# Optimization experiments

Hardware: AMD Instinct MI355X
Metric: run time of the kernel (lower is better)

Reference implementation:

```python
import jax, jax.numpy as jnp
import numpy as np

N, IN_CH, HID, HEADS, OUT_CH, E = 30000, 256, 128, 4, 256, 480000
NEG_SLOPE = 0.2  # PyG GATConv default LeakyReLU slope


def setup_inputs() -> dict:
    key = jax.random.key(0)
    ks = jax.random.split(key, 12)
    s = lambda fin: 1.0 / np.sqrt(fin)
    return {
        "x": jax.random.normal(ks[0], (N, IN_CH), jnp.float32),
        "edge_index": jax.random.randint(ks[1], (2, E), 0, N, jnp.int32),
        "W1": jax.random.normal(ks[2], (IN_CH, HEADS * HID), jnp.float32) * s(IN_CH),
        "a_src1": jax.random.normal(ks[3], (HEADS, HID), jnp.float32) * s(HID),
        "a_dst1": jax.random.normal(ks[4], (HEADS, HID), jnp.float32) * s(HID),
        "b1": jnp.zeros((HEADS * HID,), jnp.float32),
        "prelu_w": jnp.asarray(0.25, jnp.float32),
        "W2": jax.random.normal(ks[5], (HEADS * HID, OUT_CH), jnp.float32) * s(HEADS * HID),
        "a_src2": jax.random.normal(ks[6], (1, OUT_CH), jnp.float32) * s(OUT_CH),
        "a_dst2": jax.random.normal(ks[7], (1, OUT_CH), jnp.float32) * s(OUT_CH),
        "b2": jnp.zeros((OUT_CH,), jnp.float32),
    }


def gat_conv(x, W, a_src, a_dst, bias, src, dst, heads, out_ch, concat):
    n = x.shape[0]
    h = (x @ W).reshape(n, heads, out_ch)                 # [n,H,C]
    al_s = jnp.einsum("nhc,hc->nh", h, a_src)             # [n,H]
    al_d = jnp.einsum("nhc,hc->nh", h, a_dst)
    logits = jax.nn.leaky_relu(al_s[src] + al_d[dst], NEG_SLOPE)  # [Et,H]
    m = jax.lax.stop_gradient(jax.ops.segment_max(logits, dst, num_segments=n))
    e = jnp.exp(logits - m[dst])
    denom = jax.ops.segment_sum(e, dst, num_segments=n)
    alpha = e / denom[dst]                                # per-dst softmax
    msg = h[src] * alpha[:, :, None]                      # [Et,H,C]
    out = jax.ops.segment_sum(msg, dst, num_segments=n)   # [n,H,C]
    out = out.reshape(n, heads * out_ch) if concat else out.mean(axis=1)
    return out + bias


def reference(x, edge_index, W1, a_src1, a_dst1, b1, prelu_w, W2, a_src2, a_dst2, b2):
    n = x.shape[0]
    loop = jnp.arange(n, dtype=edge_index.dtype)
    src = jnp.concatenate([edge_index[0], loop])          # PyG adds self-loops
    dst = jnp.concatenate([edge_index[1], loop])
    h = gat_conv(x, W1, a_src1, a_dst1, b1, src, dst, HEADS, HID, concat=True)
    h = jnp.where(h >= 0, h, prelu_w * h)                 # PReLU (eval: dropout off)
    z = gat_conv(h, W2, a_src2, a_dst2, b2, src, dst, 1, OUT_CH, concat=False)
    return z
```

## Files before the change

kernel.cpp:

```cpp
#include <hip/hip_runtime.h>
#include <hip/hip_bf16.h>
#include <float.h>

#define N_NODES 30000
#define IN_CH   256
#define HID     128
#define HEADS   4
#define OUT_CH  256
#define N_EDGES 480000
#define TOT_E   (N_EDGES + N_NODES)

typedef unsigned short u16;
typedef __attribute__((ext_vector_type(8))) unsigned short u16x8;
typedef __attribute__((ext_vector_type(8))) short          s16x8;
typedef __attribute__((ext_vector_type(4))) float          f32x4;

__device__ inline float bf2f(u16 u) {
    union { unsigned int i; float f; } v; v.i = ((unsigned int)u) << 16; return v.f;
}
__device__ inline u16 f2bf(float f) {
    union { float f; unsigned int i; } u; u.f = f;
    unsigned int r = u.i + 0x7FFF + ((u.i >> 16) & 1);
    return (u16)(r >> 16);
}

__device__ inline void load4(const float* p, float* o) {
    float4 v = *(const float4*)p; o[0]=v.x; o[1]=v.y; o[2]=v.z; o[3]=v.w;
}
__device__ inline void store4f(float* p, float a, float b, float c, float d) {
    *(float4*)p = make_float4(a,b,c,d);
}
__device__ inline void store4b(u16* p, float a, float b, float c, float d) {
    ushort4 o; o.x=f2bf(a); o.y=f2bf(b); o.z=f2bf(c); o.w=f2bf(d);
    *(ushort4*)p = o;
}

__global__ void detect_k(const unsigned int* __restrict__ w, int* __restrict__ flag) {
    __shared__ int votes;
    if (threadIdx.x == 0) votes = 0;
    __syncthreads();
    int v = 0;
    for (int i = threadIdx.x; i < 2048; i += 256) {
        unsigned int e = (w[i] >> 7) & 0xFFu;
        if (e >= 100u && e <= 140u) v++;
    }
    atomicAdd(&votes, v);
    __syncthreads();
    if (threadIdx.x == 0) *flag = (votes > 1024) ? 1 : 0;
}

__global__ void convert_bf_k(const void* __restrict__ in, u16* __restrict__ out,
                             int n, const int* __restrict__ flag) {
    int i = blockIdx.x * blockDim.x + threadIdx.x;
    if (i >= n) return;
    if (*flag) out[i] = ((const u16*)in)[i];
    else       out[i] = f2bf(((const float*)in)[i]);
}

__global__ void convert_tr_k(const void* __restrict__ in, u16* __restrict__ out,
                             int rows, int cols, const int* __restrict__ flag) {
    int i = blockIdx.x * blockDim.x + threadIdx.x;
    if (i >= rows * cols) return;
    int r = i / cols, c = i - r * cols;
    u16 v = (*flag) ? ((const u16*)in)[i] : f2bf(((const float*)in)[i]);
    out[(size_t)c * rows + r] = v;
}

__global__ void convert_small_k(const void* __restrict__ as1, const void* __restrict__ ad1,
                                const void* __restrict__ b1,  const void* __restrict__ as2,
                                const void* __restrict__ ad2, const void* __restrict__ b2,
                                const void* __restrict__ pw,
                                float* __restrict__ as1f, float* __restrict__ ad1f,
                                float* __restrict__ b1f,  float* __restrict__ as2f,
                                float* __restrict__ ad2f, float* __restrict__ b2f,
                                float* __restrict__ pwf,
                                const int* __restrict__ flag)
{
    int i = blockIdx.x * blockDim.x + threadIdx.x;
    int f = *flag;
#define CV(in, k) (f ? bf2f(((const u16*)(in))[k]) : ((const float*)(in))[k])
    if      (i < 512)  as1f[i]        = CV(as1, i);
    else if (i < 1024) ad1f[i - 512]  = CV(ad1, i - 512);
    else if (i < 1536) b1f [i - 1024] = CV(b1,  i - 1024);
    else if (i < 1792) as2f[i - 1536] = CV(as2, i - 1536);
    else if (i < 2048) ad2f[i - 1792] = CV(ad2, i - 1792);
    else if (i < 2304) b2f [i - 2048] = CV(b2,  i - 2048);
    else if (i == 2304) pwf[0]        = CV(pw, 0);
#undef CV
}

__global__ __launch_bounds__(256) void gemm_bf_k(const u16* __restrict__ A,
                                                 const u16* __restrict__ Bt,
                                                 u16* __restrict__ Cb,
                                                 const float* __restrict__ a_s,
                                                 const float* __restrict__ a_d,
                                                 float* __restrict__ als,
                                                 float* __restrict__ ald,
                                                 int M, int N, int K,
                                                 int H, int hshift)
{
    __shared__ __align__(16) u16 As[128][40];
    __shared__ __align__(16) u16 Bs[128][40];

    const int tid  = threadIdx.x;
    const int wid  = tid >> 6;
    const int lane = tid & 63;
    const int wr   = wid >> 1;
    const int wc   = wid & 1;
    const int lr   = lane & 15;
    const int lg   = lane >> 4;
    const int row0 = blockIdx.y * 128;
    const int col0 = blockIdx.x * 128;

    const int st_r = tid >> 1;
    const int st_c = (tid & 1) << 4;

    f32x4 acc[4][4];
#pragma unroll
    for (int i = 0; i < 4; ++i)
#pragma unroll
        for (int j = 0; j < 4; ++j)
            acc[i][j] = (f32x4){0.f, 0.f, 0.f, 0.f};

    for (int k0 = 0; k0 < K; k0 += 32) {
        __syncthreads();
        {
            u16x8 a0 = {}, a1 = {};
            int ar = row0 + st_r;
            if (ar < M) {
                const u16* ap = A + (size_t)ar * K + k0 + st_c;
                a0 = *(const u16x8*)ap;
                a1 = *(const u16x8*)(ap + 8);
            }
            *(u16x8*)&As[st_r][st_c]     = a0;
            *(u16x8*)&As[st_r][st_c + 8] = a1;
            const u16* bp = Bt + (size_t)(col0 + st_r) * K + k0 + st_c;
            *(u16x8*)&Bs[st_r][st_c]     = *(const u16x8*)bp;
            *(u16x8*)&Bs[st_r][st_c + 8] = *(const u16x8*)(bp + 8);
        }
        __syncthreads();

        s16x8 af[4], bf[4];
#pragma unroll
        for (int mf = 0; mf < 4; ++mf)
            af[mf] = *(const s16x8*)&As[wr*64 + mf*16 + lr][lg*8];
#pragma unroll
        for (int nf = 0; nf < 4; ++nf)
            bf[nf] = *(const s16x8*)&Bs[wc*64 + nf*16 + lr][lg*8];
#pragma unroll
        for (int mf = 0; mf < 4; ++mf)
#pragma unroll
            for (int nf = 0; nf < 4; ++nf)
                acc[mf][nf] = __builtin_amdgcn_mfma_f32_16x16x32_bf16(
                    af[mf], bf[nf], acc[mf][nf], 0, 0, 0);
    }

    const int head = (col0 + wc*64) >> hshift;
    float asj[4], adj[4];
#pragma unroll
    for (int nf = 0; nf < 4; ++nf) {
        int j = col0 + wc*64 + nf*16 + lr;
        asj[nf] = a_s[j];
        adj[nf] = a_d[j];
    }
#pragma unroll
    for (int mf = 0; mf < 4; ++mf) {
#pragma unroll
        for (int r = 0; r < 4; ++r) {
            int rr = row0 + wr*64 + mf*16 + lg*4 + r;
            float ss = 0.f, sd = 0.f;
#pragma unroll
            for (int nf = 0; nf < 4; ++nf) {
                float v = acc[mf][nf][r];
                ss += v * asj[nf];
                sd += v * adj[nf];
            }
#pragma unroll
            for (int m2 = 1; m2 < 16; m2 <<= 1) {
                ss += __shfl_xor(ss, m2);
                sd += __shfl_xor(sd, m2);
            }
            if (rr < M) {
                if (lr == 0) {
                    atomicAdd(&als[(size_t)rr * H + head], ss);
                    atomicAdd(&ald[(size_t)rr * H + head], sd);
                }
                size_t base = (size_t)rr * N + col0 + wc*64 + lr;
#pragma unroll
                for (int nf = 0; nf < 4; ++nf)
                    Cb[base + nf*16] = f2bf(acc[mf][nf][r]);
            }
        }
    }
}

__global__ void zero_k(int* p, int n) {
    int i = blockIdx.x*blockDim.x + threadIdx.x; if (i < n) p[i] = 0;
}
__global__ void count_k(const int* __restrict__ ei, int* __restrict__ cnt) {
    int i = blockIdx.x*blockDim.x + threadIdx.x;
    if (i >= TOT_E) return;
    int d = (i < N_EDGES) ? ei[N_EDGES + i] : (i - N_EDGES);
    atomicAdd(&cnt[d], 1);
}
__global__ __launch_bounds__(1024) void scan1_k(const int* __restrict__ cnt,
                                                int* __restrict__ offs,
                                                int* __restrict__ btot)
{
    __shared__ int sm[1024];
    int tid = threadIdx.x;
    int i = blockIdx.x * 1024 + tid;
    int v = (i < N_NODES) ? cnt[i] : 0;
    sm[tid] = v;
    __syncthreads();
    for (int off = 1; off < 1024; off <<= 1) {
        int t = (tid >= off) ? sm[tid - off] : 0;
        __syncthreads();
        sm[tid] += t;
        __syncthreads();
    }
    if (i < N_NODES) offs[i + 1] = sm[tid];
    if (tid == 1023) btot[blockIdx.x] = sm[1023];
}
__global__ void scan2_k(const int* __restrict__ btot, int* __restrict__ bpref, int nb)
{
    int lane = threadIdx.x;
    int orig = (lane < nb) ? btot[lane] : 0;
    int v = orig;
    for (int off = 1; off < 64; off <<= 1) {
        int t = __shfl_up(v, off);
        if (lane >= off) v += t;
    }
    if (lane < nb) bpref[lane] = v - orig;
}
__global__ __launch_bounds__(1024) void scan3_k(const int* __restrict__ cnt,
                                                int* __restrict__ offs,
                                                int* __restrict__ cursor,
                                                const int* __restrict__ bpref)
{
    int i = blockIdx.x * 1024 + threadIdx.x;
    if (i < N_NODES) {
        int inc = offs[i + 1] + bpref[blockIdx.x];
        offs[i + 1] = inc;
        cursor[i]   = inc - cnt[i];
    }
    if (i == 0) offs[0] = 0;
}
__global__ void scatter_k(const int* __restrict__ ei, int* __restrict__ cursor,
                          int* __restrict__ ssrc)
{
    int i = blockIdx.x*blockDim.x + threadIdx.x;
    if (i >= TOT_E) return;
    int s, d;
    if (i < N_EDGES) { s = ei[i]; d = ei[N_EDGES + i]; }
    else             { s = i - N_EDGES; d = s; }
    int pos = atomicAdd(&cursor[d], 1);
    ssrc[pos] = s;
}

template<int H, int C, bool PRELU, int OUTMODE>
__global__ void aggregate_k(const u16* __restrict__ hb,
                            const float* __restrict__ als,
                            const float* __restrict__ ald,
                            const int* __restrict__ offs,
                            const int* __restrict__ ssrc,
                            const float* __restrict__ bias,
                            const float* __restrict__ prelu_w,
                            void* __restrict__ outv,
                            const int* __restrict__ flag)
{
    constexpr int CT = H * C;
    constexpr int T  = CT / 4;
    constexpr int NW = T / 64;
    int n   = blockIdx.x;
    int tid = threadIdx.x;
    int beg = offs[n], end = offs[n+1];

    __shared__ float s_ald[H], s_m[H], s_inv[H];
    __shared__ float red[H][NW];
    __shared__ int   sh_s[T];
    __shared__ float sh_w[H][T];

    if (tid < H) s_ald[tid] = ald[(size_t)n*H + tid];
    __syncthreads();

    float lmax[H];
#pragma unroll
    for (int hh = 0; hh < H; ++hh) lmax[hh] = -FLT_MAX;
    for (int e = beg + tid; e < end; e += T) {
        int s = ssrc[e];
#pragma unroll
        for (int hh = 0; hh < H; ++hh) {
            float l = als[(size_t)s*H + hh] + s_ald[hh];
            l = (l >= 0.f) ? l : 0.2f*l;
            lmax[hh] = fmaxf(lmax[hh], l);
        }
    }
#pragma unroll
    for (int hh = 0; hh < H; ++hh) {
        float v = lmax[hh];
#pragma unroll
        for (int o = 32; o > 0; o >>= 1) v = fmaxf(v, __shfl_xor(v, o));
        if ((tid & 63) == 0) red[hh][tid >> 6] = v;
    }
    __syncthreads();
    if (tid < H) {
        float v = red[tid][0];
#pragma unroll
        for (int w2 = 1; w2 < NW; ++w2) v = fmaxf(v, red[tid][w2]);
        s_m[tid] = v;
    }
    __syncthreads();

    float lsum[H];
#pragma unroll
    for (int hh = 0; hh < H; ++hh) lsum[hh] = 0.f;
    for (int e = beg + tid; e < end; e += T) {
        int s = ssrc[e];
#pragma unroll
        for (int hh = 0; hh < H; ++hh) {
            float l = als[(size_t)s*H + hh] + s_ald[hh];
            l = (l >= 0.f) ? l : 0.2f*l;
            lsum[hh] += __expf(l - s_m[hh]);
        }
    }
#pragma unroll
    for (int hh = 0; hh < H; ++hh) {
        float v = lsum[hh];
#pragma unroll
        for (int o = 32; o > 0; o >>= 1) v += __shfl_xor(v, o);
        if ((tid & 63) == 0) red[hh][tid >> 6] = v;
    }
    __syncthreads();
    if (tid < H) {
        float v = 0.f;
#pragma unroll
        for (int w2 = 0; w2 < NW; ++w2) v += red[tid][w2];
        s_inv[tid] = 1.0f / v;
    }
    __syncthreads();

    const int hh = (4*tid) / C;
    float ax = 0.f, ay = 0.f, az = 0.f, aw = 0.f;
    for (int chunk = beg; chunk < end; chunk += T) {
        int e = chunk + tid;
        if (e < end) {
            int s = ssrc[e];
            sh_s[tid] = s;
#pragma unroll
            for (int h2 = 0; h2 < H; ++h2) {
                float l = als[(size_t)s*H + h2] + s_ald[h2];
                l = (l >= 0.f) ? l : 0.2f*l;
                sh_w[h2][tid] = __expf(l - s_m[h2]) * s_inv[h2];
            }
        }
        __syncthreads();
        int cnt = min(T, end - chunk);
        int j = 0;
        for (; j + 4 <= cnt; j += 4) {
            int s0 = sh_s[j+0], s1 = sh_s[j+1], s2 = sh_s[j+2], s3 = sh_s[j+3];
            float w0 = sh_w[hh][j+0], w1 = sh_w[hh][j+1];
            float w2 = sh_w[hh][j+2], w3 = sh_w[hh][j+3];
            ushort4 v0 = *(const ushort4*)(hb + (size_t)s0*CT + 4*tid);
            ushort4 v1 = *(const ushort4*)(hb + (size_t)s1*CT + 4*tid);
            ushort4 v2 = *(const ushort4*)(hb + (size_t)s2*CT + 4*tid);
            ushort4 v3 = *(const ushort4*)(hb + (size_t)s3*CT + 4*tid);
            ax += w0*bf2f(v0.x); ay += w0*bf2f(v0.y); az += w0*bf2f(v0.z); aw += w0*bf2f(v0.w);
            ax += w1*bf2f(v1.x); ay += w1*bf2f(v1.y); az += w1*bf2f(v1.z); aw += w1*bf2f(v1.w);
            ax += w2*bf2f(v2.x); ay += w2*bf2f(v2.y); az += w2*bf2f(v2.z); aw += w2*bf2f(v2.w);
            ax += w3*bf2f(v3.x); ay += w3*bf2f(v3.y); az += w3*bf2f(v3.z); aw += w3*bf2f(v3.w);
        }
        for (; j < cnt; ++j) {
            int s0 = sh_s[j];
            float w0 = sh_w[hh][j];
            ushort4 v0 = *(const ushort4*)(hb + (size_t)s0*CT + 4*tid);
            ax += w0*bf2f(v0.x); ay += w0*bf2f(v0.y); az += w0*bf2f(v0.z); aw += w0*bf2f(v0.w);
        }
        __syncthreads();
    }

    float bb[4];
    load4(bias + 4*tid, bb);
    ax += bb[0]; ay += bb[1]; az += bb[2]; aw += bb[3];
    if (PRELU) {
        float pw = *prelu_w;
        ax = ax >= 0.f ? ax : pw*ax;
        ay = ay >= 0.f ? ay : pw*ay;
        az = az >= 0.f ? az : pw*az;
        aw = aw >= 0.f ? aw : pw*aw;
    }
    size_t ofs = (size_t)n*CT + 4*tid;
    if (OUTMODE == 2) {
        if (*flag) store4b((u16*)outv + ofs, ax, ay, az, aw);
        else       store4f((float*)outv + ofs, ax, ay, az, aw);
    } else if (OUTMODE == 1) {
        store4b((u16*)outv + ofs, ax, ay, az, aw);
    } else {
        store4f((float*)outv + ofs, ax, ay, az, aw);
    }
}

extern "C" void kernel_launch(void* const* d_in, const int* in_sizes, int n_in,
                              void* d_out, int out_size, void* d_ws, size_t ws_size,
                              hipStream_t stream)
{
    const void* x   = d_in[0];
    const int*  ei  = (const int*)d_in[1];
    const void* W1  = d_in[2];
    const void* as1 = d_in[3];
    const void* ad1 = d_in[4];
    const void* b1  = d_in[5];
    const void* pw  = d_in[6];
    const void* W2  = d_in[7];
    const void* as2 = d_in[8];
    const void* ad2 = d_in[9];
    const void* b2  = d_in[10];

    float* ws = (float*)d_ws;
    int*   flag = (int*)ws;
    float* as1f = ws + 16;
    float* ad1f = as1f + 512;
    float* b1f  = ad1f + 512;
    float* as2f = b1f  + 512;
    float* ad2f = as2f + 256;
    float* b2f  = ad2f + 256;
    float* pwf  = b2f  + 256;
    u16*   W1t  = (u16*)(pwf + 16);
    u16*   W2t  = W1t + IN_CH*HEADS*HID;
    float* als1 = (float*)(W2t + HEADS*HID*OUT_CH);
    float* ald1 = als1 + (size_t)N_NODES*HEADS;
    float* als2v = ald1 + (size_t)N_NODES*HEADS;
    float* ald2v = als2v + N_NODES;
    int*   cnt    = (int*)(ald2v + N_NODES);
    int*   offs   = cnt + N_NODES;
    int*   cursor = offs + 30004;
    int*   btot   = cursor + N_NODES;
    int*   bpref  = btot + 32;
    int*   ssrc   = bpref + 36;
    u16*   xb     = (u16*)(ssrc + 510004);
    u16*   h1b    = xb  + (size_t)N_NODES*IN_CH;
    u16*   h1pb   = h1b + (size_t)N_NODES*512;
    u16*   h2b    = h1b;

    const int NB = (N_NODES + 1023) / 1024;

    detect_k<<<1, 256, 0, stream>>>((const unsigned int*)x, flag);
    convert_bf_k<<<(N_NODES*IN_CH+255)/256, 256, 0, stream>>>(x, xb, N_NODES*IN_CH, flag);
    convert_tr_k<<<(IN_CH*HEADS*HID+255)/256, 256, 0, stream>>>(W1, W1t, IN_CH, HEADS*HID, flag);
    convert_tr_k<<<(HEADS*HID*OUT_CH+255)/256, 256, 0, stream>>>(W2, W2t, HEADS*HID, OUT_CH, flag);
    convert_small_k<<<10, 256, 0, stream>>>(as1, ad1, b1, as2, ad2, b2, pw,
                                            as1f, ad1f, b1f, as2f, ad2f, b2f, pwf, flag);

    zero_k<<<(330000+255)/256, 256, 0, stream>>>((int*)als1, 330000);

    count_k  <<<(TOT_E+255)/256, 256, 0, stream>>>(ei, cnt);
    scan1_k  <<<NB, 1024, 0, stream>>>(cnt, offs, btot);
    scan2_k  <<<1, 64, 0, stream>>>(btot, bpref, NB);
    scan3_k  <<<NB, 1024, 0, stream>>>(cnt, offs, cursor, bpref);
    scatter_k<<<(TOT_E+255)/256, 256, 0, stream>>>(ei, cursor, ssrc);

    dim3 g1(512/128, (N_NODES+127)/128);
    gemm_bf_k<<<g1, 256, 0, stream>>>(xb, W1t, h1b, as1f, ad1f, als1, ald1,
                                      N_NODES, 512, IN_CH, HEADS, 7);
    aggregate_k<HEADS, HID, true, 1>
        <<<N_NODES, (HEADS*HID)/4, 0, stream>>>(h1b, als1, ald1, offs, ssrc, b1f, pwf, h1pb, flag);

    dim3 g2(256/128, (N_NODES+127)/128);
    gemm_bf_k<<<g2, 256, 0, stream>>>(h1pb, W2t, h2b, as2f, ad2f, als2v, ald2v,
                                      N_NODES, OUT_CH, HEADS*HID, 1, 8);
    aggregate_k<1, OUT_CH, false, 2>
        <<<N_NODES, OUT_CH/4, 0, stream>>>(h2b, als2v, ald2v, offs, ssrc, b2f, nullptr, d_out, flag);
}
```

Before: 375.7 us.

## Split GAT aggregation into softmax-weight precompute and channel-group gather kernels

Replaces the fused per-node aggregation kernel with two kernels. The first computes normalized attention weights per edge with one wavefront per node and writes them to a workspace buffer. The second launches one block per node and channel group, with two waves splitting the edges and scalar bf16 loads per lane. The aim is more parallelism and less per-block synchronisation, at the cost of an extra weight-buffer round-trip through memory and narrower (2-byte) gather loads.

```diff
diff --git a/kernel.cpp b/kernel.cpp
--- a/kernel.cpp
+++ b/kernel.cpp
@@ -22,17 +22,6 @@
     union { float f; unsigned int i; } u; u.f = f;
     unsigned int r = u.i + 0x7FFF + ((u.i >> 16) & 1);
     return (u16)(r >> 16);
-}
-
-__device__ inline void load4(const float* p, float* o) {
-    float4 v = *(const float4*)p; o[0]=v.x; o[1]=v.y; o[2]=v.z; o[3]=v.w;
-}
-__device__ inline void store4f(float* p, float a, float b, float c, float d) {
-    *(float4*)p = make_float4(a,b,c,d);
-}
-__device__ inline void store4b(u16* p, float a, float b, float c, float d) {
-    ushort4 o; o.x=f2bf(a); o.y=f2bf(b); o.z=f2bf(c); o.w=f2bf(d);
-    *(ushort4*)p = o;
 }
 
 __global__ void detect_k(const unsigned int* __restrict__ w, int* __restrict__ flag) {
@@ -258,145 +247,120 @@
     ssrc[pos] = s;
 }
 
-template<int H, int C, bool PRELU, int OUTMODE>
-__global__ void aggregate_k(const u16* __restrict__ hb,
-                            const float* __restrict__ als,
-                            const float* __restrict__ ald,
-                            const int* __restrict__ offs,
-                            const int* __restrict__ ssrc,
-                            const float* __restrict__ bias,
-                            const float* __restrict__ prelu_w,
-                            void* __restrict__ outv,
-                            const int* __restrict__ flag)
-{
-    constexpr int CT = H * C;
-    constexpr int T  = CT / 4;
-    constexpr int NW = T / 64;
-    int n   = blockIdx.x;
-    int tid = threadIdx.x;
+template<int H>
+__global__ __launch_bounds__(64) void softmax_prep_k(
+    const float* __restrict__ als, const float* __restrict__ ald,
+    const int* __restrict__ offs, const int* __restrict__ ssrc,
+    float* __restrict__ wbuf)
+{
+    int n = blockIdx.x;
+    int lane = threadIdx.x;
     int beg = offs[n], end = offs[n+1];
-
-    __shared__ float s_ald[H], s_m[H], s_inv[H];
-    __shared__ float red[H][NW];
-    __shared__ int   sh_s[T];
-    __shared__ float sh_w[H][T];
-
-    if (tid < H) s_ald[tid] = ald[(size_t)n*H + tid];
+    float aldh[H];
+#pragma unroll
+    for (int h = 0; h < H; ++h) aldh[h] = ald[(size_t)n*H + h];
+
+    float lmax[H];
+#pragma unroll
+    for (int h = 0; h < H; ++h) lmax[h] = -FLT_MAX;
+    for (int e = beg + lane; e < end; e += 64) {
+        int s = ssrc[e];
+#pragma unroll
+        for (int h = 0; h < H; ++h) {
+            float l = als[(size_t)s*H + h] + aldh[h];
+            l = (l >= 0.f) ? l : 0.2f*l;
+            lmax[h] = fmaxf(lmax[h], l);
+        }
+    }
+#pragma unroll
+    for (int h = 0; h < H; ++h)
+#pragma unroll
+        for (int o = 32; o > 0; o >>= 1)
+            lmax[h] = fmaxf(lmax[h], __shfl_xor(lmax[h], o));
+
+    float lsum[H];
+#pragma unroll
+    for (int h = 0; h < H; ++h) lsum[h] = 0.f;
+    for (int e = beg + lane; e < end; e += 64) {
+        int s = ssrc[e];
+#pragma unroll
+        for (int h = 0; h < H; ++h) {
+            float l = als[(size_t)s*H + h] + aldh[h];
+            l = (l >= 0.f) ? l : 0.2f*l;
+            lsum[h] += __expf(l - lmax[h]);
+        }
+    }
+#pragma unroll
+    for (int h = 0; h < H; ++h)
+#pragma unroll
+        for (int o = 32; o > 0; o >>= 1)
+            lsum[h] += __shfl_xor(lsum[h], o);
+
+    float inv[H];
+#pragma unroll
+    for (int h = 0; h < H; ++h) inv[h] = 1.0f / lsum[h];
+
+    for (int e = beg + lane; e < end; e += 64) {
+        int s = ssrc[e];
+#pragma unroll
+        for (int h = 0; h < H; ++h) {
+            float l = als[(size_t)s*H + h] + aldh[h];
+            l = (l >= 0.f) ? l : 0.2f*l;
+            wbuf[(size_t)e*H + h] = __expf(l - lmax[h]) * inv[h];
+        }
+    }
+}
+
+template<int H, int CT, int NG, bool PRELU, int OUTMODE>
+__global__ __launch_bounds__(128) void gather_k(
+    const u16* __restrict__ hb, const float* __restrict__ wbuf,
+    const int* __restrict__ offs, const int* __restrict__ ssrc,
+    const float* __restrict__ bias, const float* __restrict__ prelu_w,
+    void* __restrict__ outv, const int* __restrict__ flag)
+{
+    constexpr int CPG = CT / NG;
+    const int bid  = blockIdx.x;
+    const int g    = bid % NG;
+    const int n    = bid / NG;
+    const int wv   = threadIdx.x >> 6;
+    const int lane = threadIdx.x & 63;
+    const int c    = g * CPG + lane;
+    const int h    = c / (CT / H);
+    const int beg = offs[n], end = offs[n+1];
+
+    __shared__ float part[2][CPG];
+
+    float acc = 0.f;
+    int e = beg + wv;
+    for (; e + 6 < end; e += 8) {
+        int   s0 = ssrc[e],   s1 = ssrc[e+2], s2 = ssrc[e+4], s3 = ssrc[e+6];
+        float w0 = wbuf[(size_t)(e+0)*H + h], w1 = wbuf[(size_t)(e+2)*H + h];
+        float w2 = wbuf[(size_t)(e+4)*H + h], w3 = wbuf[(size_t)(e+6)*H + h];
+        float v0 = bf2f(hb[(size_t)s0*CT + c]);
+        float v1 = bf2f(hb[(size_t)s1*CT + c]);
+        float v2 = bf2f(hb[(size_t)s2*CT + c]);
+        float v3 = bf2f(hb[(size_t)s3*CT + c]);
+        acc += w0*v0 + w1*v1 + w2*v2 + w3*v3;
+    }
+    for (; e < end; e += 2) {
+        int s0 = ssrc[e];
+        float w0 = wbuf[(size_t)e*H + h];
+        acc += w0 * bf2f(hb[(size_t)s0*CT + c]);
+    }
+    part[wv][lane] = acc;
     __syncthreads();
-
-    float lmax[H];
-#pragma unroll
-    for (int hh = 0; hh < H; ++hh) lmax[hh] = -FLT_MAX;
-    for (int e = beg + tid; e < end; e += T) {
-        int s = ssrc[e];
-#pragma unroll
-        for (int hh = 0; hh < H; ++hh) {
-            float l = als[(size_t)s*H + hh] + s_ald[hh];
-            l = (l >= 0.f) ? l : 0.2f*l;
-            lmax[hh] = fmaxf(lmax[hh], l);
-        }
-    }
-#pragma unroll
-    for (int hh = 0; hh < H; ++hh) {
-        float v = lmax[hh];
-#pragma unroll
-        for (int o = 32; o > 0; o >>= 1) v = fmaxf(v, __shfl_xor(v, o));
-        if ((tid & 63) == 0) red[hh][tid >> 6] = v;
-    }
-    __syncthreads();
-    if (tid < H) {
-        float v = red[tid][0];
-#pragma unroll
-        for (int w2 = 1; w2 < NW; ++w2) v = fmaxf(v, red[tid][w2]);
-        s_m[tid] = v;
-    }
-    __syncthreads();
-
-    float lsum[H];
-#pragma unroll
-    for (int hh = 0; hh < H; ++hh) lsum[hh] = 0.f;
-    for (int e = beg + tid; e < end; e += T) {
-        int s = ssrc[e];
-#pragma unroll
-        for (int hh = 0; hh < H; ++hh) {
-            float l = als[(size_t)s*H + hh] + s_ald[hh];
-            l = (l >= 0.f) ? l : 0.2f*l;
-            lsum[hh] += __expf(l - s_m[hh]);
-        }
-    }
-#pragma unroll
-    for (int hh = 0; hh < H; ++hh) {
-        float v = lsum[hh];
-#pragma unroll
-        for (int o = 32; o > 0; o >>= 1) v += __shfl_xor(v, o);
-        if ((tid & 63) == 0) red[hh][tid >> 6] = v;
-    }
-    __syncthreads();
-    if (tid < H) {
-        float v = 0.f;
-#pragma unroll
-        for (int w2 = 0; w2 < NW; ++w2) v += red[tid][w2];
-        s_inv[tid] = 1.0f / v;
-    }
-    __syncthreads();
-
-    const int hh = (4*tid) / C;
-    float ax = 0.f, ay = 0.f, az = 0.f, aw = 0.f;
-    for (int chunk = beg; chunk < end; chunk += T) {
-        int e = chunk + tid;
-        if (e < end) {
-            int s = ssrc[e];
-            sh_s[tid] = s;
-#pragma unroll
-            for (int h2 = 0; h2 < H; ++h2) {
-                float l = als[(size_t)s*H + h2] + s_ald[h2];
-                l = (l >= 0.f) ? l : 0.2f*l;
-                sh_w[h2][tid] = __expf(l - s_m[h2]) * s_inv[h2];
-            }
-        }
-        __syncthreads();
-        int cnt = min(T, end - chunk);
-        int j = 0;
-        for (; j + 4 <= cnt; j += 4) {
-            int s0 = sh_s[j+0], s1 = sh_s[j+1], s2 = sh_s[j+2], s3 = sh_s[j+3];
-            float w0 = sh_w[hh][j+0], w1 = sh_w[hh][j+1];
-            float w2 = sh_w[hh][j+2], w3 = sh_w[hh][j+3];
-            ushort4 v0 = *(const ushort4*)(hb + (size_t)s0*CT + 4*tid);
-            ushort4 v1 = *(const ushort4*)(hb + (size_t)s1*CT + 4*tid);
-            ushort4 v2 = *(const ushort4*)(hb + (size_t)s2*CT + 4*tid);
-            ushort4 v3 = *(const ushort4*)(hb + (size_t)s3*CT + 4*tid);
-            ax += w0*bf2f(v0.x); ay += w0*bf2f(v0.y); az += w0*bf2f(v0.z); aw += w0*bf2f(v0.w);
-            ax += w1*bf2f(v1.x); ay += w1*bf2f(v1.y); az += w1*bf2f(v1.z); aw += w1*bf2f(v1.w);
-            ax += w2*bf2f(v2.x); ay += w2*bf2f(v2.y); az += w2*bf2f(v2.z); aw += w2*bf2f(v2.w);
-            ax += w3*bf2f(v3.x); ay += w3*bf2f(v3.y); az += w3*bf2f(v3.z); aw += w3*bf2f(v3.w);
-        }
-        for (; j < cnt; ++j) {
-            int s0 = sh_s[j];
-            float w0 = sh_w[hh][j];
-            ushort4 v0 = *(const ushort4*)(hb + (size_t)s0*CT + 4*tid);
-            ax += w0*bf2f(v0.x); ay += w0*bf2f(v0.y); az += w0*bf2f(v0.z); aw += w0*bf2f(v0.w);
-        }
-        __syncthreads();
-    }
-
-    float bb[4];
-    load4(bias + 4*tid, bb);
-    ax += bb[0]; ay += bb[1]; az += bb[2]; aw += bb[3];
-    if (PRELU) {
-        float pw = *prelu_w;
-        ax = ax >= 0.f ? ax : pw*ax;
-        ay = ay >= 0.f ? ay : pw*ay;
-        az = az >= 0.f ? az : pw*az;
-        aw = aw >= 0.f ? aw : pw*aw;
-    }
-    size_t ofs = (size_t)n*CT + 4*tid;
-    if (OUTMODE == 2) {
-        if (*flag) store4b((u16*)outv + ofs, ax, ay, az, aw);
-        else       store4f((float*)outv + ofs, ax, ay, az, aw);
-    } else if (OUTMODE == 1) {
-        store4b((u16*)outv + ofs, ax, ay, az, aw);
-    } else {
-        store4f((float*)outv + ofs, ax, ay, az, aw);
+    if (wv == 0) {
+        float r = part[0][lane] + part[1][lane] + bias[c];
+        if (PRELU) { float pw = *prelu_w; r = (r >= 0.f) ? r : pw * r; }
+        size_t o = (size_t)n * CT + c;
+        if (OUTMODE == 1) {
+            ((u16*)outv)[o] = f2bf(r);
+        } else if (OUTMODE == 2) {
+            if (*flag) ((u16*)outv)[o] = f2bf(r);
+            else       ((float*)outv)[o] = r;
+        } else {
+            ((float*)outv)[o] = r;
+        }
     }
 }
 
@@ -437,7 +401,8 @@
     int*   btot   = cursor + N_NODES;
     int*   bpref  = btot + 32;
     int*   ssrc   = bpref + 36;
-    u16*   xb     = (u16*)(ssrc + 510004);
+    float* wbuf   = (float*)(ssrc + 510004);
+    u16*   xb     = (u16*)(wbuf + 2040016);
     u16*   h1b    = xb  + (size_t)N_NODES*IN_CH;
     u16*   h1pb   = h1b + (size_t)N_NODES*512;
     u16*   h2b    = h1b;
@@ -462,12 +427,14 @@
     dim3 g1(512/128, (N_NODES+127)/128);
     gemm_bf_k<<<g1, 256, 0, stream>>>(xb, W1t, h1b, as1f, ad1f, als1, ald1,
                                       N_NODES, 512, IN_CH, HEADS, 7);
-    aggregate_k<HEADS, HID, true, 1>
-        <<<N_NODES, (HEADS*HID)/4, 0, stream>>>(h1b, als1, ald1, offs, ssrc, b1f, pwf, h1pb, flag);
+    softmax_prep_k<HEADS><<<N_NODES, 64, 0, stream>>>(als1, ald1, offs, ssrc, wbuf);
+    gather_k<HEADS, 512, 8, true, 1>
+        <<<N_NODES*8, 128, 0, stream>>>(h1b, wbuf, offs, ssrc, b1f, pwf, h1pb, flag);
 
     dim3 g2(256/128, (N_NODES+127)/128);
     gemm_bf_k<<<g2, 256, 0, stream>>>(h1pb, W2t, h2b, as2f, ad2f, als2v, ald2v,
                                       N_NODES, OUT_CH, HEADS*HID, 1, 8);
-    aggregate_k<1, OUT_CH, false, 2>
-        <<<N_NODES, OUT_CH/4, 0, stream>>>(h2b, als2v, ald2v, offs, ssrc, b2f, nullptr, d_out, flag);
-}
+    softmax_prep_k<1><<<N_NODES, 64, 0, stream>>>(als2v, ald2v, offs, ssrc, wbuf);
+    gather_k<1, 256, 4, false, 2>
+        <<<N_NODES*4, 128, 0, stream>>>(h2b, wbuf, offs, ssrc, b2f, nullptr, d_out, flag);
+}
```

Measured after the change: 566.2 us. +50.7%, slower.

## Use single-wave aggregation blocks and drop softmax max-subtraction pass

Applied to the files above, without the earlier changes.

Rewrites the aggregation kernel so each node is handled by a single 64-thread wavefront with 8- or 4-wide bf16 vector loads. Reductions become shuffle-only with no shared-memory staging or extra barriers. The max-logit pass is removed, so the softmax exponentiates raw logits. This saves one full pass over the edge list and several block syncs, but large logits could overflow exp, and each node gets fewer threads for the gather.

```diff
diff --git a/kernel.cpp b/kernel.cpp
--- a/kernel.cpp
+++ b/kernel.cpp
@@ -22,17 +22,6 @@
     union { float f; unsigned int i; } u; u.f = f;
     unsigned int r = u.i + 0x7FFF + ((u.i >> 16) & 1);
     return (u16)(r >> 16);
-}
-
-__device__ inline void load4(const float* p, float* o) {
-    float4 v = *(const float4*)p; o[0]=v.x; o[1]=v.y; o[2]=v.z; o[3]=v.w;
-}
-__device__ inline void store4f(float* p, float a, float b, float c, float d) {
-    *(float4*)p = make_float4(a,b,c,d);
-}
-__device__ inline void store4b(u16* p, float a, float b, float c, float d) {
-    ushort4 o; o.x=f2bf(a); o.y=f2bf(b); o.z=f2bf(c); o.w=f2bf(d);
-    *(ushort4*)p = o;
 }
 
 __global__ void detect_k(const unsigned int* __restrict__ w, int* __restrict__ flag) {
@@ -258,145 +247,137 @@
     ssrc[pos] = s;
 }
 
-template<int H, int C, bool PRELU, int OUTMODE>
-__global__ void aggregate_k(const u16* __restrict__ hb,
-                            const float* __restrict__ als,
-                            const float* __restrict__ ald,
-                            const int* __restrict__ offs,
-                            const int* __restrict__ ssrc,
-                            const float* __restrict__ bias,
-                            const float* __restrict__ prelu_w,
-                            void* __restrict__ outv,
-                            const int* __restrict__ flag)
+template<int H, int C, int VW, bool PRELU, int OUTMODE>
+__global__ __launch_bounds__(64) void aggregate_k(
+    const u16* __restrict__ hb,
+    const float* __restrict__ als,
+    const float* __restrict__ ald,
+    const int* __restrict__ offs,
+    const int* __restrict__ ssrc,
+    const float* __restrict__ bias,
+    const float* __restrict__ prelu_w,
+    void* __restrict__ outv,
+    const int* __restrict__ flag)
 {
     constexpr int CT = H * C;
-    constexpr int T  = CT / 4;
-    constexpr int NW = T / 64;
-    int n   = blockIdx.x;
-    int tid = threadIdx.x;
-    int beg = offs[n], end = offs[n+1];
-
-    __shared__ float s_ald[H], s_m[H], s_inv[H];
-    __shared__ float red[H][NW];
+    constexpr int T  = 64;
+    static_assert(CT == T * VW, "geometry");
+    const int n   = blockIdx.x;
+    const int tid = threadIdx.x;
+    const int beg = offs[n], end = offs[n+1];
+
+    float aldh[H];
+#pragma unroll
+    for (int h = 0; h < H; ++h) aldh[h] = ald[(size_t)n*H + h];
+
+    float lsum[H];
+#pragma unroll
+    for (int h = 0; h < H; ++h) lsum[h] = 0.f;
+    for (int e = beg + tid; e < end; e += T) {
+        int s = ssrc[e];
+#pragma unroll
+        for (int h = 0; h < H; ++h) {
+            float l = als[(size_t)s*H + h] + aldh[h];
+            l = (l >= 0.f) ? l : 0.2f*l;
+            lsum[h] += __expf(l);
+        }
+    }
+#pragma unroll
+    for (int h = 0; h < H; ++h) {
+#pragma unroll
+        for (int o = 32; o > 0; o >>= 1) lsum[h] += __shfl_xor(lsum[h], o);
+    }
+    float inv[H];
+#pragma unroll
+    for (int h = 0; h < H; ++h) inv[h] = 1.0f / lsum[h];
+
     __shared__ int   sh_s[T];
     __shared__ float sh_w[H][T];
-
-    if (tid < H) s_ald[tid] = ald[(size_t)n*H + tid];
-    __syncthreads();
-
-    float lmax[H];
-#pragma unroll
-    for (int hh = 0; hh < H; ++hh) lmax[hh] = -FLT_MAX;
-    for (int e = beg + tid; e < end; e += T) {
-        int s = ssrc[e];
-#pragma unroll
-        for (int hh = 0; hh < H; ++hh) {
-            float l = als[(size_t)s*H + hh] + s_ald[hh];
-            l = (l >= 0.f) ? l : 0.2f*l;
-            lmax[hh] = fmaxf(lmax[hh], l);
-        }
-    }
-#pragma unroll
-    for (int hh = 0; hh < H; ++hh) {
-        float v = lmax[hh];
-#pragma unroll
-        for (int o = 32; o > 0; o >>= 1) v = fmaxf(v, __shfl_xor(v, o));
-        if ((tid & 63) == 0) red[hh][tid >> 6] = v;
-    }
-    __syncthreads();
-    if (tid < H) {
-        float v = red[tid][0];
-#pragma unroll
-        for (int w2 = 1; w2 < NW; ++w2) v = fmaxf(v, red[tid][w2]);
-        s_m[tid] = v;
-    }
-    __syncthreads();
-
-    float lsum[H];
-#pragma unroll
-    for (int hh = 0; hh < H; ++hh) lsum[hh] = 0.f;
-    for (int e = beg + tid; e < end; e += T) {
-        int s = ssrc[e];
-#pragma unroll
-        for (int hh = 0; hh < H; ++hh) {
-            float l = als[(size_t)s*H + hh] + s_ald[hh];
-            l = (l >= 0.f) ? l : 0.2f*l;
-            lsum[hh] += __expf(l - s_m[hh]);
-        }
-    }
-#pragma unroll
-    for (int hh = 0; hh < H; ++hh) {
-        float v = lsum[hh];
-#pragma unroll
-        for (int o = 32; o > 0; o >>= 1) v += __shfl_xor(v, o);
-        if ((tid & 63) == 0) red[hh][tid >> 6] = v;
-    }
-    __syncthreads();
-    if (tid < H) {
-        float v = 0.f;
-#pragma unroll
-        for (int w2 = 0; w2 < NW; ++w2) v += red[tid][w2];
-        s_inv[tid] = 1.0f / v;
-    }
-    __syncthreads();
-
-    const int hh = (4*tid) / C;
-    float ax = 0.f, ay = 0.f, az = 0.f, aw = 0.f;
+    const int hh = (VW * tid) / C;
+    float acc[VW];
+#pragma unroll
+    for (int k = 0; k < VW; ++k) acc[k] = 0.f;
+
     for (int chunk = beg; chunk < end; chunk += T) {
         int e = chunk + tid;
         if (e < end) {
             int s = ssrc[e];
             sh_s[tid] = s;
 #pragma unroll
-            for (int h2 = 0; h2 < H; ++h2) {
-                float l = als[(size_t)s*H + h2] + s_ald[h2];
+            for (int h = 0; h < H; ++h) {
+                float l = als[(size_t)s*H + h] + aldh[h];
                 l = (l >= 0.f) ? l : 0.2f*l;
-                sh_w[h2][tid] = __expf(l - s_m[h2]) * s_inv[h2];
+                sh_w[h][tid] = __expf(l) * inv[h];
             }
         }
         __syncthreads();
         int cnt = min(T, end - chunk);
         int j = 0;
         for (; j + 4 <= cnt; j += 4) {
-            int s0 = sh_s[j+0], s1 = sh_s[j+1], s2 = sh_s[j+2], s3 = sh_s[j+3];
+            int   s0 = sh_s[j+0], s1 = sh_s[j+1], s2 = sh_s[j+2], s3 = sh_s[j+3];
             float w0 = sh_w[hh][j+0], w1 = sh_w[hh][j+1];
             float w2 = sh_w[hh][j+2], w3 = sh_w[hh][j+3];
-            ushort4 v0 = *(const ushort4*)(hb + (size_t)s0*CT + 4*tid);
-            ushort4 v1 = *(const ushort4*)(hb + (size_t)s1*CT + 4*tid);
-            ushort4 v2 = *(const ushort4*)(hb + (size_t)s2*CT + 4*tid);
-            ushort4 v3 = *(const ushort4*)(hb + (size_t)s3*CT + 4*tid);
-            ax += w0*bf2f(v0.x); ay += w0*bf2f(v0.y); az += w0*bf2f(v0.z); aw += w0*bf2f(v0.w);
-            ax += w1*bf2f(v1.x); ay += w1*bf2f(v1.y); az += w1*bf2f(v1.z); aw += w1*bf2f(v1.w);
-            ax += w2*bf2f(v2.x); ay += w2*bf2f(v2.y); az += w2*bf2f(v2.z); aw += w2*bf2f(v2.w);
-            ax += w3*bf2f(v3.x); ay += w3*bf2f(v3.y); az += w3*bf2f(v3.z); aw += w3*bf2f(v3.w);
+            if constexpr (VW == 8) {
+                u16x8 v0 = *(const u16x8*)(hb + (size_t)s0*CT + VW*tid);
+                u16x8 v1 = *(const u16x8*)(hb + (size_t)s1*CT + VW*tid);
+                u16x8 v2 = *(const u16x8*)(hb + (size_t)s2*CT + VW*tid);
+                u16x8 v3 = *(const u16x8*)(hb + (size_t)s3*CT + VW*tid);
+#pragma unroll
+                for (int k = 0; k < 8; ++k) {
+                    acc[k] += w0*bf2f(v0[k]) + w1*bf2f(v1[k])
+                            + w2*bf2f(v2[k]) + w3*bf2f(v3[k]);
+                }
+            } else {
+                ushort4 v0 = *(const ushort4*)(hb + (size_t)s0*CT + VW*tid);
+                ushort4 v1 = *(const ushort4*)(hb + (size_t)s1*CT + VW*tid);
+                ushort4 v2 = *(const ushort4*)(hb + (size_t)s2*CT + VW*tid);
+                ushort4 v3 = *(const ushort4*)(hb + (size_t)s3*CT + VW*tid);
+                acc[0] += w0*bf2f(v0.x) + w1*bf2f(v1.x) + w2*bf2f(v2.x) + w3*bf2f(v3.x);
+                acc[1] += w0*bf2f(v0.y) + w1*bf2f(v1.y) + w2*bf2f(v2.y) + w3*bf2f(v3.y);
+                acc[2] += w0*bf2f(v0.z) + w1*bf2f(v1.z) + w2*bf2f(v2.z) + w3*bf2f(v3.z);
+                acc[3] += w0*bf2f(v0.w) + w1*bf2f(v1.w) + w2*bf2f(v2.w) + w3*bf2f(v3.w);
+            }
         }
         for (; j < cnt; ++j) {
             int s0 = sh_s[j];
             float w0 = sh_w[hh][j];
-            ushort4 v0 = *(const ushort4*)(hb + (size_t)s0*CT + 4*tid);
-            ax += w0*bf2f(v0.x); ay += w0*bf2f(v0.y); az += w0*bf2f(v0.z); aw += w0*bf2f(v0.w);
-        }
-        __syncthreads();
-    }
-
-    float bb[4];
-    load4(bias + 4*tid, bb);
-    ax += bb[0]; ay += bb[1]; az += bb[2]; aw += bb[3];
+            if constexpr (VW == 8) {
+                u16x8 v0 = *(const u16x8*)(hb + (size_t)s0*CT + VW*tid);
+#pragma unroll
+                for (int k = 0; k < 8; ++k) acc[k] += w0*bf2f(v0[k]);
+            } else {
+                ushort4 v0 = *(const ushort4*)(hb + (size_t)s0*CT + VW*tid);
+                acc[0] += w0*bf2f(v0.x); acc[1] += w0*bf2f(v0.y);
+                acc[2] += w0*bf2f(v0.z); acc[3] += w0*bf2f(v0.w);
+            }
+        }
+        __syncthreads();
+    }
+
+#pragma unroll
+    for (int k = 0; k < VW; ++k) acc[k] += bias[VW*tid + k];
     if (PRELU) {
         float pw = *prelu_w;
-        ax = ax >= 0.f ? ax : pw*ax;
-        ay = ay >= 0.f ? ay : pw*ay;
-        az = az >= 0.f ? az : pw*az;
-        aw = aw >= 0.f ? aw : pw*aw;
-    }
-    size_t ofs = (size_t)n*CT + 4*tid;
-    if (OUTMODE == 2) {
-        if (*flag) store4b((u16*)outv + ofs, ax, ay, az, aw);
-        else       store4f((float*)outv + ofs, ax, ay, az, aw);
-    } else if (OUTMODE == 1) {
-        store4b((u16*)outv + ofs, ax, ay, az, aw);
+#pragma unroll
+        for (int k = 0; k < VW; ++k) acc[k] = (acc[k] >= 0.f) ? acc[k] : pw*acc[k];
+    }
+    size_t ofs = (size_t)n*CT + VW*tid;
+    bool bf = (OUTMODE == 1) || (OUTMODE == 2 && *flag);
+    if (bf) {
+        if constexpr (VW == 8) {
+            u16x8 o;
+#pragma unroll
+            for (int k = 0; k < 8; ++k) o[k] = f2bf(acc[k]);
+            *(u16x8*)((u16*)outv + ofs) = o;
+        } else {
+            ushort4 o; o.x=f2bf(acc[0]); o.y=f2bf(acc[1]); o.z=f2bf(acc[2]); o.w=f2bf(acc[3]);
+            *(ushort4*)((u16*)outv + ofs) = o;
+        }
     } else {
-        store4f((float*)outv + ofs, ax, ay, az, aw);
+        float* op = (float*)outv + ofs;
+#pragma unroll
+        for (int k = 0; k < VW; k += 4)
+            *(float4*)(op + k) = make_float4(acc[k], acc[k+1], acc[k+2], acc[k+3]);
     }
 }
 
@@ -462,12 +443,12 @@
     dim3 g1(512/128, (N_NODES+127)/128);
     gemm_bf_k<<<g1, 256, 0, stream>>>(xb, W1t, h1b, as1f, ad1f, als1, ald1,
                                       N_NODES, 512, IN_CH, HEADS, 7);
-    aggregate_k<HEADS, HID, true, 1>
-        <<<N_NODES, (HEADS*HID)/4, 0, stream>>>(h1b, als1, ald1, offs, ssrc, b1f, pwf, h1pb, flag);
+    aggregate_k<HEADS, HID, 8, true, 1>
+        <<<N_NODES, 64, 0, stream>>>(h1b, als1, ald1, offs, ssrc, b1f, pwf, h1pb, flag);
 
     dim3 g2(256/128, (N_NODES+127)/128);
     gemm_bf_k<<<g2, 256, 0, stream>>>(h1pb, W2t, h2b, as2f, ad2f, als2v, ald2v,
                                       N_NODES, OUT_CH, HEADS*HID, 1, 8);
-    aggregate_k<1, OUT_CH, false, 2>
-        <<<N_NODES, OUT_CH/4, 0, stream>>>(h2b, als2v, ald2v, offs, ssrc, b2f, nullptr, d_out, flag);
-}
+    aggregate_k<1, OUT_CH, 4, false, 2>
+        <<<N_NODES, 64, 0, stream>>>(h2b, als2v, ald2v, offs, ssrc, b2f, nullptr, d_out, flag);
+}
```

New measurement: 361.8 us. -3.7%, faster.
